# Optimization experiments

Measured on AMD Instinct MI355X. Metric: run time of the kernel, lower is better.

The kernel has to match this reference:

```python
import jax, jax.numpy as jnp
import numpy as np

B, L, DIM, H = 2, 2048, 2048, 16
D = DIM // H
EPS = 1e-6
CAP = 50.0
SCALE = D ** -0.5


def _rms_norm(x, w):
    # x: [B,H,L,D], normalize over last dim
    scale = jax.lax.rsqrt(jnp.maximum(jnp.mean(x * x, axis=-1, keepdims=True), EPS))
    return w * x * scale


def _rotate_half(x):
    x1, x2 = jnp.split(x, 2, axis=-1)
    return jnp.concatenate([-x2, x1], axis=-1)


def setup_inputs() -> dict:
    key = jax.random.key(0)
    ks = jax.random.split(key, 6)
    x = jax.random.normal(ks[0], (B, L, DIM), dtype=jnp.float32)
    w_qkv = jax.random.normal(ks[1], (3 * DIM, DIM), dtype=jnp.float32) * (DIM ** -0.5)
    w_out = jax.random.normal(ks[2], (DIM, DIM), dtype=jnp.float32) * (DIM ** -0.5)
    q_norm_w = jnp.ones((D,), dtype=jnp.float32)
    k_norm_w = jnp.ones((D,), dtype=jnp.float32)
    # rope tables [L, D]
    inv_freq = 1.0 / (10000.0 ** (np.arange(0, D, 2, dtype=np.float32) / D))
    t = np.arange(L, dtype=np.float32)
    freqs = np.outer(t, inv_freq)  # [L, D/2]
    emb = np.concatenate([freqs, freqs], axis=-1)  # [L, D]
    cos = jnp.asarray(np.cos(emb), dtype=jnp.float32)
    sin = jnp.asarray(np.sin(emb), dtype=jnp.float32)
    # additive causal mask [1,1,L,L]
    causal = np.triu(np.full((L, L), -1e9, dtype=np.float32), k=1)
    mask = jnp.asarray(causal)[None, None]
    return {"x": x, "w_qkv": w_qkv, "w_out": w_out, "q_norm_w": q_norm_w,
            "k_norm_w": k_norm_w, "cos": cos, "sin": sin, "mask": mask}


def reference(x, w_qkv, w_out, q_norm_w, k_norm_w, cos, sin, mask):
    b, l, _ = x.shape
    qkv = jnp.einsum('bld,ed->ble', x, w_qkv).reshape(b, l, 3, H, D)
    q, k, v = [jnp.transpose(qkv[:, :, i], (0, 2, 1, 3)) for i in range(3)]  # [B,H,L,D]
    q = _rms_norm(q, q_norm_w)
    k = _rms_norm(k, k_norm_w)
    # rope: cos/sin are [L,D] -> [1,1,L,D]
    c = cos[-l:, :][None, None]
    s = sin[-l:, :][None, None]
    q = q * c + _rotate_half(q) * s
    k = k * c + _rotate_half(k) * s
    attn = jnp.einsum('bhqd,bhkd->bhqk', q, k) * SCALE
    attn = jnp.tanh(attn / CAP) * CAP + mask
    probs = jax.nn.softmax(attn, axis=-1)
    o = jnp.einsum('bhqk,bhkd->bhqd', probs, v)
    o = jnp.transpose(o, (0, 2, 1, 3)).reshape(b, l, H * D)
    out = jnp.einsum('bld,ed->ble', o, w_out)
    return (out, (k, v))
```

## Files before the change

kernel.cpp:

```cpp
#include <hip/hip_runtime.h>
#include <hip/hip_bf16.h>
#include <stdint.h>

#define LL 2048
#define DD 128
#define HH 16

typedef float f32x4 __attribute__((ext_vector_type(4)));
typedef float f32x2 __attribute__((ext_vector_type(2)));
typedef short bf16x8 __attribute__((ext_vector_type(8)));
typedef short short4v __attribute__((ext_vector_type(4)));
typedef float float4v __attribute__((ext_vector_type(4)));

__device__ __forceinline__ float bf2f(short s) {
  union { unsigned u; float f; } v; v.u = ((unsigned)(unsigned short)s) << 16; return v.f;
}
__device__ __forceinline__ short f2bf(float f) {
  union { float f; unsigned u; } v; v.f = f;
  unsigned u = v.u;
  u += 0x7fffu + ((u >> 16) & 1u);
  return (short)(u >> 16);
}

__device__ __forceinline__ void gload_lds16(const void* g, void* lds) {
  __builtin_amdgcn_global_load_lds(
      (__attribute__((address_space(1))) unsigned int*)(void*)(uintptr_t)g,
      (__attribute__((address_space(3))) unsigned int*)lds, 16, 0, 0);
}

__global__ __launch_bounds__(256) void cast_all_kernel(
    const float* __restrict__ x, const float* __restrict__ wqkv,
    const float* __restrict__ wout, short* __restrict__ dst)
{
  long i4 = ((long)blockIdx.x * 256 + threadIdx.x) * 4;
  const float* src; long off;
  if (i4 < 8388608L)        { src = x;    off = i4; }
  else if (i4 < 20971520L)  { src = wqkv; off = i4 - 8388608L; }
  else                      { src = wout; off = i4 - 20971520L; }
  float4v v = *(const float4v*)(src + off);
  short4v o;
  o.x = f2bf(v.x); o.y = f2bf(v.y); o.z = f2bf(v.z); o.w = f2bf(v.w);
  *(short4v*)(dst + i4) = o;
}

#define SCHED __builtin_amdgcn_sched_barrier(0)
#define BARRIER { SCHED; __builtin_amdgcn_s_barrier(); SCHED; }

#define STAGE(buf, opx, ptr, rb, ks, t)                                        \
  { _Pragma("unroll") for (int l_ = 0; l_ < 2; ++l_) {                          \
      int ch_ = l_ * 512 + tid;                                                 \
      int row_ = ch_ >> 2, ci_ = ch_ & 3;                                       \
      gload_lds16(ptr + (size_t)(rb + row_) * K + (t) * 64 + (ks) * 32 +        \
                      ((ci_ ^ (row_ & 3)) << 3),                                \
                  &lds[buf][opx][ks][ch_ << 3]);                                \
  } }

#define LDA(buf, mh, ks)                                                       \
  { _Pragma("unroll") for (int mf_ = 0; mf_ < 4; ++mf_) {                       \
      int r_ = wm * 128 + (mh) * 64 + mf_ * 16 + j;                             \
      areg[mf_] = *(const bf16x8*)&lds[buf][0][ks][r_ * 32 + ((g ^ (j & 3)) << 3)]; \
  } }

#define LDB(dst, buf, ks)                                                      \
  { _Pragma("unroll") for (int nf_ = 0; nf_ < 4; ++nf_) {                       \
      int r_ = wn * 64 + nf_ * 16 + j;                                          \
      dst[nf_] = *(const bf16x8*)&lds[buf][1][ks][r_ * 32 + ((g ^ (j & 3)) << 3)]; \
  } }

#define MFMAQ(mh, breg)                                                        \
  { __builtin_amdgcn_s_setprio(1);                                             \
    _Pragma("unroll") for (int mf_ = 0; mf_ < 4; ++mf_)                         \
      _Pragma("unroll") for (int nf_ = 0; nf_ < 4; ++nf_)                       \
        acc[(mh) * 4 + mf_][nf_] = __builtin_amdgcn_mfma_f32_16x16x32_bf16(     \
            areg[mf_], breg[nf_], acc[(mh) * 4 + mf_][nf_], 0, 0, 0);           \
    __builtin_amdgcn_s_setprio(0); }

__global__ __launch_bounds__(512, 2) void gemm256_kernel(
    const short* __restrict__ A, const short* __restrict__ Bm,
    short* __restrict__ C, int M, int N, int K)
{
  __shared__ __align__(16) short lds[2][2][2][8192];
  const int tid = threadIdx.x;
  const int lane = tid & 63;
  const int wid = tid >> 6;
  const int wm = wid >> 2, wn = wid & 3;
  const int g = lane >> 4, j = lane & 15;
  const int m0 = blockIdx.y * 256, n0 = blockIdx.x * 256;
  const int NT = K >> 6;

  f32x4 acc[8][4];
  const f32x4 z = {0.f, 0.f, 0.f, 0.f};
#pragma unroll
  for (int im = 0; im < 8; ++im)
#pragma unroll
    for (int nf = 0; nf < 4; ++nf) acc[im][nf] = z;

  STAGE(0, 1, Bm, n0, 0, 0); STAGE(0, 1, Bm, n0, 1, 0);
  STAGE(0, 0, A,  m0, 0, 0); STAGE(0, 0, A,  m0, 1, 0);
  STAGE(1, 1, Bm, n0, 0, 1); STAGE(1, 1, Bm, n0, 1, 1);
  STAGE(1, 0, A,  m0, 0, 1);
  asm volatile("s_waitcnt vmcnt(6)" ::: "memory");
  __builtin_amdgcn_s_barrier();
  SCHED;

  bf16x8 areg[4], b0r[4], b1r[4];
#pragma unroll 1
  for (int i = 0; i < (NT >> 1) - 1; ++i) {
    int t0 = i * 2;
    LDA(0, 0, 0); LDB(b0r, 0, 0);
    STAGE(1, 0, A, m0, 1, t0 + 1);
    BARRIER; MFMAQ(0, b0r); BARRIER;
    LDA(0, 0, 1); LDB(b1r, 0, 1);
    STAGE(0, 1, Bm, n0, 0, t0 + 2);
    BARRIER; MFMAQ(0, b1r); BARRIER;
    LDA(0, 1, 0);
    STAGE(0, 1, Bm, n0, 1, t0 + 2);
    BARRIER; MFMAQ(1, b0r); BARRIER;
    LDA(0, 1, 1);
    STAGE(0, 0, A, m0, 0, t0 + 2);
    BARRIER; MFMAQ(1, b1r);
    SCHED; asm volatile("s_waitcnt vmcnt(6)" ::: "memory");
    __builtin_amdgcn_s_barrier(); SCHED;
    LDA(1, 0, 0); LDB(b0r, 1, 0);
    STAGE(0, 0, A, m0, 1, t0 + 2);
    BARRIER; MFMAQ(0, b0r); BARRIER;
    LDA(1, 0, 1); LDB(b1r, 1, 1);
    STAGE(1, 1, Bm, n0, 0, t0 + 3);
    BARRIER; MFMAQ(0, b1r); BARRIER;
    LDA(1, 1, 0);
    STAGE(1, 1, Bm, n0, 1, t0 + 3);
    BARRIER; MFMAQ(1, b0r); BARRIER;
    LDA(1, 1, 1);
    STAGE(1, 0, A, m0, 0, t0 + 3);
    BARRIER; MFMAQ(1, b1r);
    SCHED; asm volatile("s_waitcnt vmcnt(6)" ::: "memory");
    __builtin_amdgcn_s_barrier(); SCHED;
  }
  {
    LDA(0, 0, 0); LDB(b0r, 0, 0);
    STAGE(1, 0, A, m0, 1, NT - 1);
    BARRIER; MFMAQ(0, b0r); BARRIER;
    LDA(0, 0, 1); LDB(b1r, 0, 1);
    BARRIER; MFMAQ(0, b1r); BARRIER;
    LDA(0, 1, 0);
    BARRIER; MFMAQ(1, b0r); BARRIER;
    LDA(0, 1, 1);
    BARRIER; MFMAQ(1, b1r);
    SCHED; asm volatile("s_waitcnt vmcnt(0)" ::: "memory");
    __builtin_amdgcn_s_barrier(); SCHED;
    LDA(1, 0, 0); LDB(b0r, 1, 0); MFMAQ(0, b0r);
    LDA(1, 0, 1); LDB(b1r, 1, 1); MFMAQ(0, b1r);
    LDA(1, 1, 0); MFMAQ(1, b0r);
    LDA(1, 1, 1); MFMAQ(1, b1r);
  }
#pragma unroll
  for (int im = 0; im < 8; ++im)
#pragma unroll
    for (int nf = 0; nf < 4; ++nf)
#pragma unroll
      for (int r = 0; r < 4; ++r)
        C[(size_t)(m0 + wm * 128 + im * 16 + g * 4 + r) * N + n0 + wn * 64 + nf * 16 + j] =
            f2bf(acc[im][nf][r]);
}

template <typename OutT>
__global__ __launch_bounds__(256) void gemm_bt_kernel(
    const short* __restrict__ A, const short* __restrict__ Bm,
    OutT* __restrict__ C, int M, int N, int K)
{
  __shared__ __align__(16) short As[128 * 64];
  __shared__ __align__(16) short Bs[128 * 64];
  const int tid = threadIdx.x;
  const int lane = tid & 63;
  const int g = lane >> 4, j = lane & 15;
  const int m0 = blockIdx.y * 128, n0 = blockIdx.x * 128;
  const int wave = tid >> 6;
  const int wm = (wave >> 1) * 64, wn = (wave & 1) * 64;

  f32x4 acc[4][4];
  const f32x4 z = {0.f, 0.f, 0.f, 0.f};
#pragma unroll
  for (int i = 0; i < 4; ++i)
#pragma unroll
    for (int jj = 0; jj < 4; ++jj) acc[i][jj] = z;

  for (int k0 = 0; k0 < K; k0 += 64) {
#pragma unroll
    for (int it = 0; it < 4; ++it) {
      int c = it * 256 + tid;
      int row = c >> 3, ko = (c & 7) << 3;
      gload_lds16(A + (size_t)(m0 + row) * K + k0 + ko, As + c * 8);
    }
#pragma unroll
    for (int it = 0; it < 4; ++it) {
      int c = it * 256 + tid;
      int row = c >> 3, ko = (c & 7) << 3;
      gload_lds16(Bm + (size_t)(n0 + row) * K + k0 + ko, Bs + c * 8);
    }
    __syncthreads();
#pragma unroll
    for (int ks = 0; ks < 2; ++ks) {
      bf16x8 af[4], bfr[4];
#pragma unroll
      for (int i = 0; i < 4; ++i)
        af[i] = *(const bf16x8*)(As + (wm + i * 16 + j) * 64 + ks * 32 + g * 8);
#pragma unroll
      for (int i = 0; i < 4; ++i)
        bfr[i] = *(const bf16x8*)(Bs + (wn + i * 16 + j) * 64 + ks * 32 + g * 8);
#pragma unroll
      for (int i = 0; i < 4; ++i)
#pragma unroll
        for (int jj = 0; jj < 4; ++jj)
          acc[i][jj] = __builtin_amdgcn_mfma_f32_16x16x32_bf16(af[i], bfr[jj], acc[i][jj], 0, 0, 0);
    }
    __syncthreads();
  }
#pragma unroll
  for (int i = 0; i < 4; ++i)
#pragma unroll
    for (int jj = 0; jj < 4; ++jj)
#pragma unroll
      for (int r = 0; r < 4; ++r) {
        int row = m0 + wm + i * 16 + g * 4 + r;
        int col = n0 + wn + jj * 16 + j;
        if constexpr (sizeof(OutT) == 4)
          C[(size_t)row * N + col] = acc[i][jj][r];
        else
          C[(size_t)row * N + col] = f2bf(acc[i][jj][r]);
      }
}

__global__ __launch_bounds__(256) void normrope_kernel(
    const short* __restrict__ qkv, const float* __restrict__ qw,
    const float* __restrict__ kw, const float* __restrict__ cosb,
    const float* __restrict__ sinb, short* __restrict__ qo,
    float* __restrict__ ko, short* __restrict__ kb, float* __restrict__ vo)
{
  int wid = (blockIdx.x * 256 + threadIdx.x) >> 6;
  int lane = threadIdx.x & 63;
  int h = wid & 15;
  int rest = wid >> 4;
  int t = rest % 3;
  int bl = rest / 3;
  int l = bl & (LL - 1);
  int d0 = lane * 2;
  const short* src = qkv + (size_t)bl * 6144 + t * 2048 + h * 128 + d0;
  int raw = *(const int*)src;
  float v0 = bf2f((short)(raw & 0xffff));
  float v1 = bf2f((short)((raw >> 16) & 0xffff));
  size_t oidx = ((size_t)((bl >> 11) * HH + h) * LL + l) * DD + d0;
  if (t == 2) {
    f32x2 vv = {v0, v1};
    *(f32x2*)(vo + oidx) = vv;
    return;
  }
  float ss = v0 * v0 + v1 * v1;
#pragma unroll
  for (int m = 1; m <= 32; m <<= 1) ss += __shfl_xor(ss, m, 64);
  float scale = rsqrtf(fmaxf(ss * (1.0f / 128.0f), 1e-6f));
  const float* w = (t == 0) ? qw : kw;
  float n0 = w[d0] * v0 * scale;
  float n1 = w[d0 + 1] * v1 * scale;
  float c0 = cosb[l * 128 + d0], c1 = cosb[l * 128 + d0 + 1];
  float s0 = sinb[l * 128 + d0], s1 = sinb[l * 128 + d0 + 1];
  float p0 = __shfl_xor(n0, 32, 64);
  float p1 = __shfl_xor(n1, 32, 64);
  float r0 = (lane < 32) ? -p0 : p0;
  float r1 = (lane < 32) ? -p1 : p1;
  float o0 = n0 * c0 + r0 * s0;
  float o1 = n1 * c1 + r1 * s1;
  int pk = (int)((unsigned short)f2bf(o0) | ((unsigned)(unsigned short)f2bf(o1) << 16));
  if (t == 0) {
    *(int*)(qo + oidx) = pk;
  } else {
    f32x2 kk = {o0, o1};
    *(f32x2*)(ko + oidx) = kk;
    *(int*)(kb + oidx) = pk;
  }
}

__global__ __launch_bounds__(256) void transpose_v_kernel(
    const float* __restrict__ v, short* __restrict__ vT)
{
  __shared__ __align__(16) short tl[64 * 72];
  int bid = blockIdx.x;
  int dt = bid & 1;
  int lt = (bid >> 1) & 31;
  int bh = bid >> 6;
  int tid = threadIdx.x;
#pragma unroll
  for (int it = 0; it < 4; ++it) {
    int c = it * 256 + tid;
    int row = c >> 4, off = (c & 15) << 2;
    float4v val = *(const float4v*)(v + ((size_t)bh * LL + lt * 64 + row) * DD + dt * 64 + off);
    short4v s;
    s.x = f2bf(val.x); s.y = f2bf(val.y); s.z = f2bf(val.z); s.w = f2bf(val.w);
    *(short4v*)(tl + row * 72 + off) = s;
  }
  __syncthreads();
#pragma unroll
  for (int it = 0; it < 2; ++it) {
    int c = it * 256 + tid;
    int dr = c >> 3, lo = (c & 7) << 3;
    bf16x8 o;
#pragma unroll
    for (int i = 0; i < 8; ++i) o[i] = tl[(lo + i) * 72 + dr];
    *(bf16x8*)(vT + ((size_t)bh * DD + dt * 64 + dr) * LL + lt * 64 + lo) = o;
  }
}

__global__ __launch_bounds__(256, 2) void attn_kernel(
    const short* __restrict__ q, const short* __restrict__ k,
    const short* __restrict__ vT, short* __restrict__ o)
{
  __shared__ __align__(16) short Ks[64 * 136];
  __shared__ __align__(16) short Vs[128 * 72];
  __shared__ __align__(16) short Ps[128 * 72];
  int bid = blockIdx.x;
  int bh = bid & 31;
  int gq = (bid >> 5) & 7;
  int qt = (bid < 256) ? (15 - gq) : gq;
  int b = bh >> 4;
  int h = bh & 15;
  int tid = threadIdx.x;
  int lane = tid & 63;
  int w = tid >> 6;
  int g = lane >> 4, j = lane & 15;
  int q0 = qt * 128;
  int wrow = q0 + w * 32;

  bf16x8 qf[2][4];
#pragma unroll
  for (int mi = 0; mi < 2; ++mi)
#pragma unroll
    for (int ks = 0; ks < 4; ++ks)
      qf[mi][ks] = *(const bf16x8*)(q + ((size_t)bh * LL + wrow + mi * 16 + j) * DD + ks * 32 + g * 8);

  f32x4 accO[2][8];
  const f32x4 z = {0.f, 0.f, 0.f, 0.f};
#pragma unroll
  for (int mi = 0; mi < 2; ++mi)
#pragma unroll
    for (int n = 0; n < 8; ++n) accO[mi][n] = z;
  float lsum[2][4] = {{0.f,0.f,0.f,0.f},{0.f,0.f,0.f,0.f}};

  const float c2 = 0.0035355339059327379f;
  int ktmax = 2 * qt + 1;
  for (int kt = 0; kt <= ktmax; ++kt) {
    int k0 = kt * 64;
#pragma unroll
    for (int it = 0; it < 4; ++it) {
      int c = it * 256 + tid;
      int row = c >> 4, off = (c & 15) << 3;
      bf16x8 val = *(const bf16x8*)(k + ((size_t)bh * LL + k0 + row) * DD + off);
      *(bf16x8*)(Ks + row * 136 + off) = val;
    }
#pragma unroll
    for (int it = 0; it < 4; ++it) {
      int c = it * 256 + tid;
      int row = c >> 3, off = (c & 7) << 3;
      bf16x8 val = *(const bf16x8*)(vT + ((size_t)bh * DD + row) * LL + k0 + off);
      *(bf16x8*)(Vs + row * 72 + off) = val;
    }
    __syncthreads();

    f32x4 sa[2][4];
#pragma unroll
    for (int mi = 0; mi < 2; ++mi)
#pragma unroll
      for (int n = 0; n < 4; ++n) sa[mi][n] = z;
#pragma unroll
    for (int ks = 0; ks < 4; ++ks) {
#pragma unroll
      for (int n = 0; n < 4; ++n) {
        bf16x8 kf = *(const bf16x8*)(Ks + (n * 16 + j) * 136 + ks * 32 + g * 8);
#pragma unroll
        for (int mi = 0; mi < 2; ++mi)
          sa[mi][n] = __builtin_amdgcn_mfma_f32_16x16x32_bf16(qf[mi][ks], kf, sa[mi][n], 0, 0, 0);
      }
    }

#pragma unroll
    for (int mi = 0; mi < 2; ++mi) {
      const bool wmask = (k0 + 63) > (wrow + mi * 16);
#pragma unroll
      for (int r = 0; r < 4; ++r) {
        int row_g = wrow + mi * 16 + g * 4 + r;
#pragma unroll
        for (int n = 0; n < 4; ++n) {
          float e2 = __expf(sa[mi][n][r] * c2);
          float t = 38.f - 100.f * __builtin_amdgcn_rcpf(e2 + 1.f);
          float p = __expf(t);
          if (wmask && (k0 + n * 16 + j > row_g)) p = 0.f;
          lsum[mi][r] += p;
          Ps[(w * 32 + mi * 16 + g * 4 + r) * 72 + n * 16 + j] = f2bf(p);
        }
      }
    }
#pragma unroll
    for (int ks = 0; ks < 2; ++ks) {
      bf16x8 pf[2];
#pragma unroll
      for (int mi = 0; mi < 2; ++mi)
        pf[mi] = *(const bf16x8*)(Ps + (w * 32 + mi * 16 + j) * 72 + ks * 32 + g * 8);
#pragma unroll
      for (int n = 0; n < 8; ++n) {
        bf16x8 vf = *(const bf16x8*)(Vs + (n * 16 + j) * 72 + ks * 32 + g * 8);
#pragma unroll
        for (int mi = 0; mi < 2; ++mi)
          accO[mi][n] = __builtin_amdgcn_mfma_f32_16x16x32_bf16(pf[mi], vf, accO[mi][n], 0, 0, 0);
      }
    }
    __syncthreads();
  }

#pragma unroll
  for (int mi = 0; mi < 2; ++mi)
#pragma unroll
    for (int r = 0; r < 4; ++r) {
#pragma unroll
      for (int m = 1; m <= 8; m <<= 1) lsum[mi][r] += __shfl_xor(lsum[mi][r], m, 64);
    }

#pragma unroll
  for (int mi = 0; mi < 2; ++mi) {
    size_t obase = ((size_t)b * LL + wrow + mi * 16) * 2048 + h * 128;
#pragma unroll
    for (int r = 0; r < 4; ++r) {
      float inv = 1.f / lsum[mi][r];
#pragma unroll
      for (int n = 0; n < 8; ++n)
        o[obase + (size_t)(g * 4 + r) * 2048 + n * 16 + j] = f2bf(accO[mi][n][r] * inv);
    }
  }
}

extern "C" void kernel_launch(void* const* d_in, const int* in_sizes, int n_in,
                              void* d_out, int out_size, void* d_ws, size_t ws_size,
                              hipStream_t stream) {
  const float* x    = (const float*)d_in[0];
  const float* wqkv = (const float*)d_in[1];
  const float* wout = (const float*)d_in[2];
  const float* qw   = (const float*)d_in[3];
  const float* kw   = (const float*)d_in[4];
  const float* cosb = (const float*)d_in[5];
  const float* sinb = (const float*)d_in[6];

  float* out   = (float*)d_out;
  float* k_out = out + 8388608;
  float* v_out = out + 16777216;

  short* ws    = (short*)d_ws;
  short* xb    = ws;
  short* wqkvb = ws + 8388608;
  short* woutb = ws + 20971520;
  short* qkv   = ws + 25165824;
  short* qbuf  = xb;
  short* kbuf  = wqkvb;
  short* vT    = qkv;
  short* obuf  = qkv + 8388608;

  cast_all_kernel<<<24576, 256, 0, stream>>>(x, wqkv, wout, ws);
  gemm256_kernel<<<dim3(24, 16), 512, 0, stream>>>(xb, wqkvb, qkv, 4096, 6144, 2048);
  normrope_kernel<<<49152, 256, 0, stream>>>(qkv, qw, kw, cosb, sinb, qbuf, k_out, kbuf, v_out);
  transpose_v_kernel<<<2048, 256, 0, stream>>>(v_out, vT);
  attn_kernel<<<512, 256, 0, stream>>>(qbuf, kbuf, vT, obuf);
  gemm_bt_kernel<float><<<dim3(16, 32), 256, 0, stream>>>(obuf, woutb, out, 4096, 2048, 2048);
}
```

Baseline: 320.8 us.

## Prefetch next K/V tile into registers in attention; change GEMM LDS swizzle

The attention kernel now issues global loads for the next K and V tiles into registers before computing the current tile, and writes them to LDS after the end-of-iteration barrier. This hides global load latency behind the QK and PV MFMA work. The GEMM's LDS XOR swizzle now keys on (row>>1)&3 instead of row&3, which changes the bank-conflict pattern of the 16-byte reads. The prefetch costs extra VGPRs for kreg/vreg, which may lower occupancy.

```diff
diff --git a/kernel.cpp b/kernel.cpp
--- a/kernel.cpp
+++ b/kernel.cpp
@@ -51,20 +51,20 @@
       int ch_ = l_ * 512 + tid;                                                 \
       int row_ = ch_ >> 2, ci_ = ch_ & 3;                                       \
       gload_lds16(ptr + (size_t)(rb + row_) * K + (t) * 64 + (ks) * 32 +        \
-                      ((ci_ ^ (row_ & 3)) << 3),                                \
+                      ((ci_ ^ ((row_ >> 1) & 3)) << 3),                         \
                   &lds[buf][opx][ks][ch_ << 3]);                                \
   } }
 
 #define LDA(buf, mh, ks)                                                       \
   { _Pragma("unroll") for (int mf_ = 0; mf_ < 4; ++mf_) {                       \
       int r_ = wm * 128 + (mh) * 64 + mf_ * 16 + j;                             \
-      areg[mf_] = *(const bf16x8*)&lds[buf][0][ks][r_ * 32 + ((g ^ (j & 3)) << 3)]; \
+      areg[mf_] = *(const bf16x8*)&lds[buf][0][ks][r_ * 32 + ((g ^ ((j >> 1) & 3)) << 3)]; \
   } }
 
 #define LDB(dst, buf, ks)                                                      \
   { _Pragma("unroll") for (int nf_ = 0; nf_ < 4; ++nf_) {                       \
       int r_ = wn * 64 + nf_ * 16 + j;                                          \
-      dst[nf_] = *(const bf16x8*)&lds[buf][1][ks][r_ * 32 + ((g ^ (j & 3)) << 3)]; \
+      dst[nf_] = *(const bf16x8*)&lds[buf][1][ks][r_ * 32 + ((g ^ ((j >> 1) & 3)) << 3)]; \
   } }
 
 #define MFMAQ(mh, breg)                                                        \
@@ -329,6 +329,9 @@
   int q0 = qt * 128;
   int wrow = q0 + w * 32;
 
+  const short* kp = k + (size_t)bh * LL * DD;
+  const short* vp = vT + (size_t)bh * DD * LL;
+
   bf16x8 qf[2][4];
 #pragma unroll
   for (int mi = 0; mi < 2; ++mi)
@@ -344,25 +347,40 @@
     for (int n = 0; n < 8; ++n) accO[mi][n] = z;
   float lsum[2][4] = {{0.f,0.f,0.f,0.f},{0.f,0.f,0.f,0.f}};
 
+#pragma unroll
+  for (int it = 0; it < 4; ++it) {
+    int c = it * 256 + tid;
+    int row = c >> 4, off = (c & 15) << 3;
+    *(bf16x8*)(Ks + row * 136 + off) = *(const bf16x8*)(kp + (size_t)row * DD + off);
+  }
+#pragma unroll
+  for (int it = 0; it < 4; ++it) {
+    int c = it * 256 + tid;
+    int row = c >> 3, off = (c & 7) << 3;
+    *(bf16x8*)(Vs + row * 72 + off) = *(const bf16x8*)(vp + (size_t)row * LL + off);
+  }
+
   const float c2 = 0.0035355339059327379f;
   int ktmax = 2 * qt + 1;
+  bf16x8 kreg[4], vreg[4];
   for (int kt = 0; kt <= ktmax; ++kt) {
     int k0 = kt * 64;
-#pragma unroll
-    for (int it = 0; it < 4; ++it) {
-      int c = it * 256 + tid;
-      int row = c >> 4, off = (c & 15) << 3;
-      bf16x8 val = *(const bf16x8*)(k + ((size_t)bh * LL + k0 + row) * DD + off);
-      *(bf16x8*)(Ks + row * 136 + off) = val;
-    }
-#pragma unroll
-    for (int it = 0; it < 4; ++it) {
-      int c = it * 256 + tid;
-      int row = c >> 3, off = (c & 7) << 3;
-      bf16x8 val = *(const bf16x8*)(vT + ((size_t)bh * DD + row) * LL + k0 + off);
-      *(bf16x8*)(Vs + row * 72 + off) = val;
-    }
     __syncthreads();
+    if (kt < ktmax) {
+      int k0n = k0 + 64;
+#pragma unroll
+      for (int it = 0; it < 4; ++it) {
+        int c = it * 256 + tid;
+        int row = c >> 4, off = (c & 15) << 3;
+        kreg[it] = *(const bf16x8*)(kp + (size_t)(k0n + row) * DD + off);
+      }
+#pragma unroll
+      for (int it = 0; it < 4; ++it) {
+        int c = it * 256 + tid;
+        int row = c >> 3, off = (c & 7) << 3;
+        vreg[it] = *(const bf16x8*)(vp + (size_t)row * LL + k0n + off);
+      }
+    }
 
     f32x4 sa[2][4];
 #pragma unroll
@@ -412,6 +430,20 @@
       }
     }
     __syncthreads();
+    if (kt < ktmax) {
+#pragma unroll
+      for (int it = 0; it < 4; ++it) {
+        int c = it * 256 + tid;
+        int row = c >> 4, off = (c & 15) << 3;
+        *(bf16x8*)(Ks + row * 136 + off) = kreg[it];
+      }
+#pragma unroll
+      for (int it = 0; it < 4; ++it) {
+        int c = it * 256 + tid;
+        int row = c >> 3, off = (c & 7) << 3;
+        *(bf16x8*)(Vs + row * 72 + off) = vreg[it];
+      }
+    }
   }
 
 #pragma unroll
```

Result: no change. 320.6 us (-0.1%).
